# Performance work log

Measured on AMD Instinct MI355X. Metric: run time of the kernel, lower is better.

The kernel has to match this reference:

```python
import jax, jax.numpy as jnp
import numpy as np

N_NODES = 50000
N_EDGES = 800000
N_GRAPHS = 50
IN_FEATS = 128
H1_FEATS = 64
OUT_FEATS = 32
GAT_SLOPE = 0.2   # DGL GATConv default negative_slope
LRELU_SLOPE = 0.01  # F.leaky_relu default


def setup_inputs() -> dict:
    key = jax.random.key(0)
    ks = jax.random.split(key, 12)
    x = jax.random.normal(ks[0], (N_NODES, IN_FEATS), jnp.float32)
    src = jax.random.randint(ks[1], (N_EDGES,), 0, N_NODES)
    dst = jax.random.randint(ks[2], (N_EDGES,), 0, N_NODES)
    graph_id = jnp.sort(jax.random.randint(ks[3], (N_NODES,), 0, N_GRAPHS))
    s1 = 1.0 / np.sqrt(IN_FEATS)
    s2 = 1.0 / np.sqrt(H1_FEATS)
    W1 = jax.random.normal(ks[4], (IN_FEATS, H1_FEATS), jnp.float32) * s1
    al1 = jax.random.normal(ks[5], (H1_FEATS,), jnp.float32) * s2
    ar1 = jax.random.normal(ks[6], (H1_FEATS,), jnp.float32) * s2
    b1 = jnp.zeros((H1_FEATS,), jnp.float32)
    W2 = jax.random.normal(ks[7], (H1_FEATS, OUT_FEATS), jnp.float32) * s2
    al2 = jax.random.normal(ks[8], (OUT_FEATS,), jnp.float32) * (1.0 / np.sqrt(OUT_FEATS))
    ar2 = jax.random.normal(ks[9], (OUT_FEATS,), jnp.float32) * (1.0 / np.sqrt(OUT_FEATS))
    b2 = jnp.zeros((OUT_FEATS,), jnp.float32)
    return {"x": x, "src": src, "dst": dst, "graph_id": graph_id,
            "W1": W1, "al1": al1, "ar1": ar1, "b1": b1,
            "W2": W2, "al2": al2, "ar2": ar2, "b2": b2}


def _gat_layer(h, src, dst, W, al, ar, b, n_nodes):
    # single-head DGL GATConv (feat_drop=attn_drop=0, bias added post-aggregation)
    z = h @ W                                   # (N, out)
    el = z @ al                                 # (N,) left attention logits
    er = z @ ar                                 # (N,) right attention logits
    e = jax.nn.leaky_relu(el[src] + er[dst], GAT_SLOPE)     # (E,)
    m = jax.ops.segment_max(e, dst, num_segments=n_nodes)  # per-dst max for stable softmax
    p = jnp.exp(e - m[dst])
    s = jax.ops.segment_sum(p, dst, num_segments=n_nodes)
    alpha = p / s[dst]                          # edge softmax over incoming edges
    out = jax.ops.segment_sum(alpha[:, None] * z[src], dst, num_segments=n_nodes)
    return out + b


def reference(x, src, dst, graph_id, W1, al1, ar1, b1, W2, al2, ar2, b2):
    n = x.shape[0]
    h = jax.nn.leaky_relu(_gat_layer(x, src, dst, W1, al1, ar1, b1, n), LRELU_SLOPE)
    h = jax.nn.leaky_relu(_gat_layer(h, src, dst, W2, al2, ar2, b2, n), LRELU_SLOPE)
    # dgl.mean_nodes: per-graph mean over nodes
    cnt = jax.ops.segment_sum(jnp.ones((n,), h.dtype), graph_id, num_segments=N_GRAPHS)
    pooled = jax.ops.segment_sum(h, graph_id, num_segments=N_GRAPHS) / jnp.maximum(cnt, 1.0)[:, None]
    return pooled
```

## Files before the change

### kernel.cpp

```cpp
#include <hip/hip_runtime.h>
#include <math.h>

#define NN 50000
#define NE 800000
#define NG 50
#define F0 128
#define F1 64
#define F2 32
#define NPB 256
#define NBK 196
#define CHUNK 4096
#define NC 196

__device__ __forceinline__ float lrelu(float v, float slope) {
    return v > 0.0f ? v : v * slope;
}

__global__ __launch_bounds__(256) void gemm1_kernel(
    const float* __restrict__ x, const float* __restrict__ W,
    const float* __restrict__ al, const float* __restrict__ ar,
    float* __restrict__ z, float* __restrict__ el, float* __restrict__ er)
{
    __shared__ float Ws[F0 * F1];
    __shared__ float xs[4][F0];
    int tid = threadIdx.x;
    for (int i = tid; i < F0 * F1; i += 256) Ws[i] = W[i];
    __syncthreads();
    int wave = tid >> 6, lane = tid & 63;
    float a_l = al[lane], a_r = ar[lane];
    for (int row = blockIdx.x * 4 + wave; row < NN; row += gridDim.x * 4) {
        float2 xv = *reinterpret_cast<const float2*>(&x[row * F0 + lane * 2]);
        xs[wave][lane * 2]     = xv.x;
        xs[wave][lane * 2 + 1] = xv.y;
        float acc = 0.f;
        #pragma unroll 16
        for (int k = 0; k < F0; ++k)
            acc = fmaf(xs[wave][k], Ws[k * F1 + lane], acc);
        z[row * F1 + lane] = acc;
        float pl = acc * a_l, pr = acc * a_r;
        #pragma unroll
        for (int mm = 1; mm < 64; mm <<= 1) {
            pl += __shfl_xor(pl, mm);
            pr += __shfl_xor(pr, mm);
        }
        if (lane == 0) { el[row] = pl; er[row] = pr; }
    }
}

__global__ __launch_bounds__(256) void gemm2_kernel(
    const float* __restrict__ h, const float* __restrict__ W,
    const float* __restrict__ al, const float* __restrict__ ar,
    float* __restrict__ z, float* __restrict__ el, float* __restrict__ er)
{
    __shared__ float Ws[F1 * F2];
    __shared__ float xs[4][2 * F1];
    int tid = threadIdx.x;
    for (int i = tid; i < F1 * F2; i += 256) Ws[i] = W[i];
    __syncthreads();
    int wave = tid >> 6, lane = tid & 63;
    int half = lane >> 5, j = lane & 31;
    float a_l = al[j], a_r = ar[j];
    for (int r0 = (blockIdx.x * 4 + wave) * 2; r0 < NN; r0 += gridDim.x * 8) {
        float2 xv = *reinterpret_cast<const float2*>(&h[(size_t)r0 * F1 + lane * 2]);
        xs[wave][lane * 2]     = xv.x;
        xs[wave][lane * 2 + 1] = xv.y;
        int row = r0 + half;
        float acc = 0.f;
        #pragma unroll 16
        for (int k = 0; k < F1; ++k)
            acc = fmaf(xs[wave][half * F1 + k], Ws[k * F2 + j], acc);
        z[row * F2 + j] = acc;
        float pl = acc * a_l, pr = acc * a_r;
        #pragma unroll
        for (int mm = 1; mm < 32; mm <<= 1) {
            pl += __shfl_xor(pl, mm);
            pr += __shfl_xor(pr, mm);
        }
        if (j == 0) { el[row] = pl; er[row] = pr; }
    }
}


__global__ __launch_bounds__(256) void p1_hist_kernel(
    const int* __restrict__ dst, int* __restrict__ hist)
{
    __shared__ int h[NBK];
    int c = blockIdx.x;
    if (threadIdx.x < NBK) h[threadIdx.x] = 0;
    __syncthreads();
    int e0 = c * CHUNK;
    int e1 = (e0 + CHUNK < NE) ? e0 + CHUNK : NE;
    for (int e = e0 + threadIdx.x; e < e1; e += 256)
        atomicAdd(&h[dst[e] >> 8], 1);
    __syncthreads();
    if (threadIdx.x < NBK) hist[threadIdx.x * NC + c] = h[threadIdx.x];
}

__global__ __launch_bounds__(256) void p2a_scan_kernel(
    int* __restrict__ hist, int* __restrict__ btot)
{
    __shared__ int t[256];
    int b = blockIdx.x;
    int v = (threadIdx.x < NC) ? hist[b * NC + threadIdx.x] : 0;
    t[threadIdx.x] = v;
    __syncthreads();
    for (int off = 1; off < 256; off <<= 1) {
        int u = (threadIdx.x >= off) ? t[threadIdx.x - off] : 0;
        __syncthreads();
        t[threadIdx.x] += u;
        __syncthreads();
    }
    if (threadIdx.x < NC) hist[b * NC + threadIdx.x] = t[threadIdx.x] - v;
    if (threadIdx.x == 255) btot[b] = t[255];
}

__global__ __launch_bounds__(256) void p2b_scan_kernel(
    const int* __restrict__ btot, int* __restrict__ bstart, int* __restrict__ row_start)
{
    __shared__ int t[256];
    int v = (threadIdx.x < NBK) ? btot[threadIdx.x] : 0;
    t[threadIdx.x] = v;
    __syncthreads();
    for (int off = 1; off < 256; off <<= 1) {
        int u = (threadIdx.x >= off) ? t[threadIdx.x - off] : 0;
        __syncthreads();
        t[threadIdx.x] += u;
        __syncthreads();
    }
    if (threadIdx.x < NBK) bstart[threadIdx.x] = t[threadIdx.x] - v;
    if (threadIdx.x == NBK) bstart[NBK] = NE;
    if (threadIdx.x == 0) row_start[NN] = NE;
}

__global__ __launch_bounds__(256) void p3_part_kernel(
    const int* __restrict__ src, const int* __restrict__ dst,
    const int* __restrict__ hist, const int* __restrict__ bstart,
    int2* __restrict__ part)
{
    __shared__ int base[NBK];
    __shared__ int cnt[NBK];
    int c = blockIdx.x;
    if (threadIdx.x < NBK) {
        base[threadIdx.x] = hist[threadIdx.x * NC + c] + bstart[threadIdx.x];
        cnt[threadIdx.x] = 0;
    }
    __syncthreads();
    int e0 = c * CHUNK;
    int e1 = (e0 + CHUNK < NE) ? e0 + CHUNK : NE;
    for (int e = e0 + threadIdx.x; e < e1; e += 256) {
        int s = src[e], d = dst[e];
        int b = d >> 8;
        int r = atomicAdd(&cnt[b], 1);
        part[base[b] + r] = make_int2(s, d);
    }
}

__global__ __launch_bounds__(256) void p4_fill_kernel(
    const int2* __restrict__ part, const int* __restrict__ bstart,
    int* __restrict__ row_start, int* __restrict__ srcs)
{
    __shared__ int deg[NPB];
    __shared__ int off[NPB];
    __shared__ int cnt[NPB];
    int b = blockIdx.x;
    int lo = bstart[b], hi = bstart[b + 1];
    deg[threadIdx.x] = 0;
    cnt[threadIdx.x] = 0;
    __syncthreads();
    for (int i = lo + threadIdx.x; i < hi; i += 256)
        atomicAdd(&deg[part[i].y & (NPB - 1)], 1);
    __syncthreads();
    int v = deg[threadIdx.x];
    off[threadIdx.x] = v;
    __syncthreads();
    for (int o = 1; o < 256; o <<= 1) {
        int u = (threadIdx.x >= o) ? off[threadIdx.x - o] : 0;
        __syncthreads();
        off[threadIdx.x] += u;
        __syncthreads();
    }
    int ex = off[threadIdx.x] - v;
    __syncthreads();
    off[threadIdx.x] = ex;
    __syncthreads();
    int node = b * NPB + threadIdx.x;
    if (node < NN) row_start[node] = lo + ex;
    for (int i = lo + threadIdx.x; i < hi; i += 256) {
        int2 e = part[i];
        int n = e.y & (NPB - 1);
        int r = atomicAdd(&cnt[n], 1);
        srcs[lo + off[n] + r] = e.x;
    }
}

__global__ __launch_bounds__(256) void gat_agg64_kernel(
    const int* __restrict__ row_start, const int* __restrict__ srcs,
    const float* __restrict__ el, const float* __restrict__ er,
    const float* __restrict__ z, const float* __restrict__ b,
    float* __restrict__ out, float slope_out)
{
    int node = (blockIdx.x * 256 + threadIdx.x) >> 6;
    if (node >= NN) return;
    int lane = threadIdx.x & 63;
    int g = lane >> 4, c = lane & 15;
    int beg = row_start[node], end = row_start[node + 1];
    float erd = er[node];

    int i0 = beg + lane;
    float v0 = -INFINITY;
    if (i0 < end) v0 = lrelu(el[srcs[i0]] + erd, 0.2f);
    float lm = v0;
    for (int i = i0 + 64; i < end; i += 64)
        lm = fmaxf(lm, lrelu(el[srcs[i]] + erd, 0.2f));
    #pragma unroll
    for (int mm = 1; mm < 64; mm <<= 1) lm = fmaxf(lm, __shfl_xor(lm, mm));

    float preg = 0.f, ls = 0.f;
    if (i0 < end) { preg = __expf(v0 - lm); ls = preg; }
    for (int i = i0 + 64; i < end; i += 64)
        ls += __expf(lrelu(el[srcs[i]] + erd, 0.2f) - lm);
    #pragma unroll
    for (int mm = 1; mm < 64; mm <<= 1) ls += __shfl_xor(ls, mm);
    float inv_s = (ls > 0.f) ? 1.0f / ls : 0.f;

    const float4* z4 = reinterpret_cast<const float4*>(z);
    float4 acc = {0.f, 0.f, 0.f, 0.f};
    for (int ib = beg; ib < end; ib += 4) {
        int i = ib + g;
        int j = i - beg;
        float pv = __shfl(preg, j & 63);
        if (i < end) {
            int sn = srcs[i];
            if (j >= 64) pv = __expf(lrelu(el[sn] + erd, 0.2f) - lm);
            float alpha = pv * inv_s;
            float4 zv = z4[(size_t)sn * 16 + c];
            acc.x = fmaf(alpha, zv.x, acc.x);
            acc.y = fmaf(alpha, zv.y, acc.y);
            acc.z = fmaf(alpha, zv.z, acc.z);
            acc.w = fmaf(alpha, zv.w, acc.w);
        }
    }
    #pragma unroll
    for (int mm = 16; mm < 64; mm <<= 1) {
        acc.x += __shfl_xor(acc.x, mm);
        acc.y += __shfl_xor(acc.y, mm);
        acc.z += __shfl_xor(acc.z, mm);
        acc.w += __shfl_xor(acc.w, mm);
    }
    if (g == 0) {
        float4 bb = reinterpret_cast<const float4*>(b)[c];
        float4 o;
        o.x = lrelu(acc.x + bb.x, slope_out);
        o.y = lrelu(acc.y + bb.y, slope_out);
        o.z = lrelu(acc.z + bb.z, slope_out);
        o.w = lrelu(acc.w + bb.w, slope_out);
        reinterpret_cast<float4*>(out)[(size_t)node * 16 + c] = o;
    }
}

__global__ __launch_bounds__(256) void gat_agg32_kernel(
    const int* __restrict__ row_start, const int* __restrict__ srcs,
    const float* __restrict__ el, const float* __restrict__ er,
    const float* __restrict__ z, const float* __restrict__ b,
    float* __restrict__ out, float slope_out)
{
    int node = (blockIdx.x * 256 + threadIdx.x) >> 5;
    if (node >= NN) return;
    int sub = threadIdx.x & 31;
    int base = threadIdx.x & 32;
    int g = sub >> 3, c = sub & 7;
    int beg = row_start[node], end = row_start[node + 1];
    float erd = er[node];

    int i0 = beg + sub;
    float v0 = -INFINITY;
    if (i0 < end) v0 = lrelu(el[srcs[i0]] + erd, 0.2f);
    float lm = v0;
    for (int i = i0 + 32; i < end; i += 32)
        lm = fmaxf(lm, lrelu(el[srcs[i]] + erd, 0.2f));
    #pragma unroll
    for (int mm = 1; mm < 32; mm <<= 1) lm = fmaxf(lm, __shfl_xor(lm, mm));

    float preg = 0.f, ls = 0.f;
    if (i0 < end) { preg = __expf(v0 - lm); ls = preg; }
    for (int i = i0 + 32; i < end; i += 32)
        ls += __expf(lrelu(el[srcs[i]] + erd, 0.2f) - lm);
    #pragma unroll
    for (int mm = 1; mm < 32; mm <<= 1) ls += __shfl_xor(ls, mm);
    float inv_s = (ls > 0.f) ? 1.0f / ls : 0.f;

    const float4* z4 = reinterpret_cast<const float4*>(z);
    float4 acc = {0.f, 0.f, 0.f, 0.f};
    for (int ib = beg; ib < end; ib += 4) {
        int i = ib + g;
        int j = i - beg;
        float pv = __shfl(preg, base | (j & 31));
        if (i < end) {
            int sn = srcs[i];
            if (j >= 32) pv = __expf(lrelu(el[sn] + erd, 0.2f) - lm);
            float alpha = pv * inv_s;
            float4 zv = z4[(size_t)sn * 8 + c];
            acc.x = fmaf(alpha, zv.x, acc.x);
            acc.y = fmaf(alpha, zv.y, acc.y);
            acc.z = fmaf(alpha, zv.z, acc.z);
            acc.w = fmaf(alpha, zv.w, acc.w);
        }
    }
    #pragma unroll
    for (int mm = 8; mm < 32; mm <<= 1) {
        acc.x += __shfl_xor(acc.x, mm);
        acc.y += __shfl_xor(acc.y, mm);
        acc.z += __shfl_xor(acc.z, mm);
        acc.w += __shfl_xor(acc.w, mm);
    }
    if (g == 0) {
        float4 bb = reinterpret_cast<const float4*>(b)[c];
        float4 o;
        o.x = lrelu(acc.x + bb.x, slope_out);
        o.y = lrelu(acc.y + bb.y, slope_out);
        o.z = lrelu(acc.z + bb.z, slope_out);
        o.w = lrelu(acc.w + bb.w, slope_out);
        reinterpret_cast<float4*>(out)[(size_t)node * 8 + c] = o;
    }
}

__global__ __launch_bounds__(256) void pool_kernel(
    const float* __restrict__ h2, const int* __restrict__ gid, float* __restrict__ out)
{
    int g = blockIdx.x;
    int lo = 0, hi = NN;
    while (lo < hi) { int mid = (lo + hi) >> 1; if (gid[mid] < g) lo = mid + 1; else hi = mid; }
    int start = lo;
    hi = NN;
    while (lo < hi) { int mid = (lo + hi) >> 1; if (gid[mid] < g + 1) lo = mid + 1; else hi = mid; }
    int end = lo;

    int f = threadIdx.x & 31, r = threadIdx.x >> 5;
    float acc = 0.f;
    for (int n = start + r; n < end; n += 8) acc += h2[(size_t)n * F2 + f];
    __shared__ float red[256];
    red[threadIdx.x] = acc;
    __syncthreads();
    for (int st = 128; st >= 32; st >>= 1) {
        if (threadIdx.x < st) red[threadIdx.x] += red[threadIdx.x + st];
        __syncthreads();
    }
    if (threadIdx.x < 32) {
        float cnt = (float)(end - start);
        out[g * F2 + threadIdx.x] = red[threadIdx.x] / fmaxf(cnt, 1.0f);
    }
}

extern "C" void kernel_launch(void* const* d_in, const int* in_sizes, int n_in,
                              void* d_out, int out_size, void* d_ws, size_t ws_size,
                              hipStream_t stream)
{
    const float* x   = (const float*)d_in[0];
    const int*   src = (const int*)d_in[1];
    const int*   dst = (const int*)d_in[2];
    const int*   gid = (const int*)d_in[3];
    const float* W1  = (const float*)d_in[4];
    const float* al1 = (const float*)d_in[5];
    const float* ar1 = (const float*)d_in[6];
    const float* b1  = (const float*)d_in[7];
    const float* W2  = (const float*)d_in[8];
    const float* al2 = (const float*)d_in[9];
    const float* ar2 = (const float*)d_in[10];
    const float* b2  = (const float*)d_in[11];
    float* out = (float*)d_out;

    float* ws   = (float*)d_ws;
    float* z1   = ws;
    float* h1   = z1 + (size_t)NN * F1;
    float* z2   = h1 + (size_t)NN * F1;
    float* h2   = z2 + (size_t)NN * F2;
    float* el   = h2 + (size_t)NN * F2;
    float* er   = el + NN;
    int* row_start = (int*)(er + NN);
    int* srcs      = row_start + NN + 1;
    int* hist      = srcs + NE;
    int* btot      = hist + NBK * NC;
    int* bstart    = btot + NBK;
    int2* part = reinterpret_cast<int2*>(z1);

    p1_hist_kernel<<<NC, 256, 0, stream>>>(dst, hist);
    p2a_scan_kernel<<<NBK, 256, 0, stream>>>(hist, btot);
    p2b_scan_kernel<<<1, 256, 0, stream>>>(btot, bstart, row_start);
    p3_part_kernel<<<NC, 256, 0, stream>>>(src, dst, hist, bstart, part);
    p4_fill_kernel<<<NBK, 256, 0, stream>>>(part, bstart, row_start, srcs);

    gemm1_kernel<<<1024, 256, 0, stream>>>(x, W1, al1, ar1, z1, el, er);
    gat_agg64_kernel<<<(NN * 64 + 255) / 256, 256, 0, stream>>>(
        row_start, srcs, el, er, z1, b1, h1, 0.01f);

    gemm2_kernel<<<1024, 256, 0, stream>>>(h1, W2, al2, ar2, z2, el, er);
    gat_agg32_kernel<<<(NN * 32 + 255) / 256, 256, 0, stream>>>(
        row_start, srcs, el, er, z2, b2, h2, 0.01f);

    pool_kernel<<<NG, 256, 0, stream>>>(h2, gid, out);
}
```

Baseline: 283.4 us.

## Register-block node GEMMs over row tiles to reuse weight loads

Both dense projection kernels are restructured so that each block stages a tile of 32 or 64 input rows in shared memory with float4 loads, and each thread accumulates 8 rows for one output column. Each weight element read from LDS is now reused across 8 rows instead of 1, and the grid is sized to one tile per block instead of a grid-stride loop. This cuts LDS traffic per FMA and vectorises global loads. In exchange the kernels use more registers and more shared memory, and every block reloads the weights.

```diff
diff --git a/kernel.cpp b/kernel.cpp
--- a/kernel.cpp
+++ b/kernel.cpp
@@ -22,28 +22,56 @@
     float* __restrict__ z, float* __restrict__ el, float* __restrict__ er)
 {
     __shared__ float Ws[F0 * F1];
-    __shared__ float xs[4][F0];
+    __shared__ float xs[32][F0];
     int tid = threadIdx.x;
-    for (int i = tid; i < F0 * F1; i += 256) Ws[i] = W[i];
-    __syncthreads();
-    int wave = tid >> 6, lane = tid & 63;
-    float a_l = al[lane], a_r = ar[lane];
-    for (int row = blockIdx.x * 4 + wave; row < NN; row += gridDim.x * 4) {
-        float2 xv = *reinterpret_cast<const float2*>(&x[row * F0 + lane * 2]);
-        xs[wave][lane * 2]     = xv.x;
-        xs[wave][lane * 2 + 1] = xv.y;
-        float acc = 0.f;
-        #pragma unroll 16
-        for (int k = 0; k < F0; ++k)
-            acc = fmaf(xs[wave][k], Ws[k * F1 + lane], acc);
-        z[row * F1 + lane] = acc;
-        float pl = acc * a_l, pr = acc * a_r;
+    int r0 = blockIdx.x * 32;
+
+    {
+        const float4* W4 = reinterpret_cast<const float4*>(W);
+        float4* Ws4 = reinterpret_cast<float4*>(Ws);
+        #pragma unroll
+        for (int i = 0; i < 8; ++i) Ws4[tid + i * 256] = W4[tid + i * 256];
+    }
+    {
+        float4 zero = {0.f, 0.f, 0.f, 0.f};
+        #pragma unroll
+        for (int i = 0; i < 4; ++i) {
+            int s = tid + i * 256;
+            int row = s >> 5, c4 = s & 31;
+            int grow = r0 + row;
+            float4 v = (grow < NN)
+                ? reinterpret_cast<const float4*>(x)[(size_t)grow * 32 + c4] : zero;
+            *reinterpret_cast<float4*>(&xs[row][c4 * 4]) = v;
+        }
+    }
+    __syncthreads();
+
+    int j = tid & 63, rg = tid >> 6;
+    float acc[8] = {0.f, 0.f, 0.f, 0.f, 0.f, 0.f, 0.f, 0.f};
+    for (int k4 = 0; k4 < F0 / 4; ++k4) {
+        float w0 = Ws[(k4 * 4 + 0) * F1 + j];
+        float w1 = Ws[(k4 * 4 + 1) * F1 + j];
+        float w2 = Ws[(k4 * 4 + 2) * F1 + j];
+        float w3 = Ws[(k4 * 4 + 3) * F1 + j];
+        #pragma unroll
+        for (int r = 0; r < 8; ++r) {
+            float4 xv = *reinterpret_cast<const float4*>(&xs[rg * 8 + r][k4 * 4]);
+            acc[r] = fmaf(xv.x, w0, fmaf(xv.y, w1, fmaf(xv.z, w2, fmaf(xv.w, w3, acc[r]))));
+        }
+    }
+
+    float a_l = al[j], a_r = ar[j];
+    #pragma unroll
+    for (int r = 0; r < 8; ++r) {
+        int row = r0 + rg * 8 + r;
+        if (row < NN) z[(size_t)row * F1 + j] = acc[r];
+        float pl = acc[r] * a_l, pr = acc[r] * a_r;
         #pragma unroll
         for (int mm = 1; mm < 64; mm <<= 1) {
             pl += __shfl_xor(pl, mm);
             pr += __shfl_xor(pr, mm);
         }
-        if (lane == 0) { el[row] = pl; er[row] = pr; }
+        if (j == 0 && row < NN) { el[row] = pl; er[row] = pr; }
     }
 }
 
@@ -53,30 +81,56 @@
     float* __restrict__ z, float* __restrict__ el, float* __restrict__ er)
 {
     __shared__ float Ws[F1 * F2];
-    __shared__ float xs[4][2 * F1];
+    __shared__ float xs[64][F1];
     int tid = threadIdx.x;
-    for (int i = tid; i < F1 * F2; i += 256) Ws[i] = W[i];
-    __syncthreads();
-    int wave = tid >> 6, lane = tid & 63;
-    int half = lane >> 5, j = lane & 31;
+    int r0 = blockIdx.x * 64;
+
+    {
+        const float4* W4 = reinterpret_cast<const float4*>(W);
+        float4* Ws4 = reinterpret_cast<float4*>(Ws);
+        #pragma unroll
+        for (int i = 0; i < 2; ++i) Ws4[tid + i * 256] = W4[tid + i * 256];
+    }
+    {
+        float4 zero = {0.f, 0.f, 0.f, 0.f};
+        #pragma unroll
+        for (int i = 0; i < 4; ++i) {
+            int s = tid + i * 256;
+            int row = s >> 4, c4 = s & 15;
+            int grow = r0 + row;
+            float4 v = (grow < NN)
+                ? reinterpret_cast<const float4*>(h)[(size_t)grow * 16 + c4] : zero;
+            *reinterpret_cast<float4*>(&xs[row][c4 * 4]) = v;
+        }
+    }
+    __syncthreads();
+
+    int j = tid & 31, rg = tid >> 5;
+    float acc[8] = {0.f, 0.f, 0.f, 0.f, 0.f, 0.f, 0.f, 0.f};
+    for (int k4 = 0; k4 < F1 / 4; ++k4) {
+        float w0 = Ws[(k4 * 4 + 0) * F2 + j];
+        float w1 = Ws[(k4 * 4 + 1) * F2 + j];
+        float w2 = Ws[(k4 * 4 + 2) * F2 + j];
+        float w3 = Ws[(k4 * 4 + 3) * F2 + j];
+        #pragma unroll
+        for (int r = 0; r < 8; ++r) {
+            float4 xv = *reinterpret_cast<const float4*>(&xs[rg * 8 + r][k4 * 4]);
+            acc[r] = fmaf(xv.x, w0, fmaf(xv.y, w1, fmaf(xv.z, w2, fmaf(xv.w, w3, acc[r]))));
+        }
+    }
+
     float a_l = al[j], a_r = ar[j];
-    for (int r0 = (blockIdx.x * 4 + wave) * 2; r0 < NN; r0 += gridDim.x * 8) {
-        float2 xv = *reinterpret_cast<const float2*>(&h[(size_t)r0 * F1 + lane * 2]);
-        xs[wave][lane * 2]     = xv.x;
-        xs[wave][lane * 2 + 1] = xv.y;
-        int row = r0 + half;
-        float acc = 0.f;
-        #pragma unroll 16
-        for (int k = 0; k < F1; ++k)
-            acc = fmaf(xs[wave][half * F1 + k], Ws[k * F2 + j], acc);
-        z[row * F2 + j] = acc;
-        float pl = acc * a_l, pr = acc * a_r;
+    #pragma unroll
+    for (int r = 0; r < 8; ++r) {
+        int row = r0 + rg * 8 + r;
+        if (row < NN) z[(size_t)row * F2 + j] = acc[r];
+        float pl = acc[r] * a_l, pr = acc[r] * a_r;
         #pragma unroll
         for (int mm = 1; mm < 32; mm <<= 1) {
             pl += __shfl_xor(pl, mm);
             pr += __shfl_xor(pr, mm);
         }
-        if (j == 0) { el[row] = pl; er[row] = pr; }
+        if (j == 0 && row < NN) { el[row] = pl; er[row] = pr; }
     }
 }
 
@@ -389,11 +443,11 @@
     p3_part_kernel<<<NC, 256, 0, stream>>>(src, dst, hist, bstart, part);
     p4_fill_kernel<<<NBK, 256, 0, stream>>>(part, bstart, row_start, srcs);
 
-    gemm1_kernel<<<1024, 256, 0, stream>>>(x, W1, al1, ar1, z1, el, er);
+    gemm1_kernel<<<(NN + 31) / 32, 256, 0, stream>>>(x, W1, al1, ar1, z1, el, er);
     gat_agg64_kernel<<<(NN * 64 + 255) / 256, 256, 0, stream>>>(
         row_start, srcs, el, er, z1, b1, h1, 0.01f);
 
-    gemm2_kernel<<<1024, 256, 0, stream>>>(h1, W2, al2, ar2, z2, el, er);
+    gemm2_kernel<<<(NN + 63) / 64, 256, 0, stream>>>(h1, W2, al2, ar2, z2, el, er);
     gat_agg32_kernel<<<(NN * 32 + 255) / 256, 256, 0, stream>>>(
         row_start, srcs, el, er, z2, b2, h2, 0.01f);
 
```

After: 286.8 us. Within noise of the previous version (+1.2%).
